# Performance work log

Hardware: AMD Instinct MI355X
Metric: run time of the kernel (lower is better)

Reference implementation:

```python
import jax, jax.numpy as jnp
import numpy as np

B, N, C, K, TOPK = 16, 4096, 256, 8, 2
EPS = 1e-6
RATIO = 0.1      # gate_geno_ratio
TEMP = 1.0       # gate_temperature


def setup_inputs() -> dict:
    key = jax.random.key(0)
    ks = jax.random.split(key, 8)
    s = np.float32(1.0 / np.sqrt(C))  # ~xavier scale for C->C linears
    return {
        "tokens": jax.random.normal(ks[0], (B, N, C), jnp.float32),
        "geno_vec": jax.random.normal(ks[1], (B, C), jnp.float32),
        # gate params (gate_proj init std=0.001; gate_geno given small random instead of exact-zero init so it contributes)
        "Wg": jax.random.normal(ks[2], (K, C), jnp.float32) * 0.001,
        "bg": jnp.zeros((K,), jnp.float32),
        "Wgg": jax.random.normal(ks[3], (K, C), jnp.float32) * 0.001,
        "bgg": jnp.zeros((K,), jnp.float32),
        # per-expert 2-layer MLP params (dropout inactive in eval)
        "W1": jax.random.normal(ks[4], (K, C, C), jnp.float32) * s,
        "b1": jnp.zeros((K, C), jnp.float32),
        "W2": jax.random.normal(ks[5], (K, C, C), jnp.float32) * s,
        "b2": jnp.zeros((K, C), jnp.float32),
    }


def reference(tokens, geno_vec, Wg, bg, Wgg, bgg, W1, b1, W2, b2):
    # gate logits: [B,N,K]
    logits = jnp.einsum("bnc,kc->bnk", tokens, Wg) + bg
    logits = logits + RATIO * (geno_vec @ Wgg.T + bgg)[:, None, :]
    logits = logits / TEMP

    topv, topi = jax.lax.top_k(logits, TOPK)          # [B,N,TOPK]
    topw = jax.nn.softmax(topv, axis=-1)
    topw = jnp.maximum(topw, EPS)
    topw = topw / topw.sum(-1, keepdims=True)

    # dense gate weight matrix W: [B,N,K] (scatter of topw at topi; topk indices are distinct)
    hot = jax.nn.one_hot(topi, K, dtype=tokens.dtype)  # [B,N,TOPK,K]
    Wmat = (hot * topw[..., None]).sum(-2)             # [B,N,K]

    # load-balance loss on hard usage (detached in original)
    usage = jax.lax.stop_gradient(hot.sum(-2).mean((0, 1)))  # [K]
    lb_loss = (jnp.std(usage) / (usage.mean() + EPS)) ** 2

    mass_sum = Wmat.sum(axis=1)                        # [B,K]

    # per-expert MLP computed densely over all tokens; zero gate weight kills
    # non-routed tokens exactly (same math as gather->MLP->scatter-add)
    def expert_center(k):
        h = jax.nn.relu(tokens @ W1[k].T + b1[k])      # [B,N,C]
        out = h @ W2[k].T + b2[k]                      # [B,N,C]
        return jnp.einsum("bn,bnc->bc", Wmat[:, :, k], out)

    centers_sum = jnp.stack([expert_center(k) for k in range(K)], axis=1)  # [B,K,C]
    centers = centers_sum / jnp.maximum(mass_sum, EPS)[..., None]

    routing_confidence = (topv[:, :, 0] - topv[:, :, 1]).mean()
    return centers, lb_loss, routing_confidence
```

## Files before the change

### kernel.cpp

```cpp
#include <hip/hip_runtime.h>

#define B_ 16
#define N_ 4096
#define C_ 256
#define K_ 8
#define EPS 1e-6f
#define RATIO 0.1f

typedef float f32x4 __attribute__((ext_vector_type(4)));
typedef __bf16 bf16x8 __attribute__((ext_vector_type(8)));

__device__ inline unsigned short f2bf(float f){
  unsigned int u = __float_as_uint(f);
  u += 0x7FFFu + ((u >> 16) & 1u);
  return (unsigned short)(u >> 16);
}
__device__ inline float bf2f(unsigned short h){
  return __uint_as_float(((unsigned int)h) << 16);
}

union BFu { ushort4 u4[2]; bf16x8 v; };

__global__ __launch_bounds__(256) void k0_prep(
    const float* __restrict__ W1, const float* __restrict__ Wg,
    const float* __restrict__ geno, const float* __restrict__ Wgg,
    const float* __restrict__ bgg,
    unsigned short* __restrict__ W1swz,
    unsigned short* __restrict__ Wgp_hi, unsigned short* __restrict__ Wgp_lo,
    int* __restrict__ cnt,
    float* __restrict__ mass, float* __restrict__ conf,
    float* __restrict__ glog)
{
  int gid = blockIdx.x * 256 + threadIdx.x;
  if (gid < B_*K_) { cnt[gid] = 0; mass[gid] = 0.f; }
  if (gid == 0) conf[0] = 0.f;
  {
    int o = gid << 3;
    int lane6 = (o >> 3) & 63;
    int s  = (o >> 9) & 7;
    int nt = (o >> 12) & 15;
    int k  = o >> 16;
    int quad = lane6 >> 4, l16 = lane6 & 15;
    int j  = nt*16 + l16;
    int c0 = s*32 + quad*8;
    const float* src = W1 + (k << 16) + (j << 8) + c0;
    unsigned short* dst = W1swz + o;
    #pragma unroll
    for (int e = 0; e < 8; ++e) dst[e] = f2bf(src[e]);
  }
  if (gid < 16*C_){
    int r = gid >> 8, c = gid & 255;
    float v = (r < K_) ? Wg[(r << 8) + c] : 0.f;
    unsigned short h = f2bf(v);
    Wgp_hi[gid] = h;
    Wgp_lo[gid] = f2bf(v - bf2f(h));
  }
  int wv = gid >> 6;
  if (wv < B_*K_){
    int lane = threadIdx.x & 63;
    int b = wv >> 3, k = wv & 7;
    float4 a = *(const float4*)(geno + b*C_ + lane*4);
    float4 w = *(const float4*)(Wgg  + k*C_ + lane*4);
    float p = a.x*w.x + a.y*w.y + a.z*w.z + a.w*w.w;
    #pragma unroll
    for (int off = 32; off; off >>= 1) p += __shfl_xor(p, off);
    if (lane == 0) glog[wv] = RATIO * (p + bgg[k]);
  }
}

__global__ __launch_bounds__(256) void k1_gate(
    const float* __restrict__ tokens,
    const unsigned short* __restrict__ Wgp_hi, const unsigned short* __restrict__ Wgp_lo,
    const float* __restrict__ bg, const float* __restrict__ glog,
    int* __restrict__ cnt, int* __restrict__ bidx, float* __restrict__ bw,
    float* __restrict__ mass, float* __restrict__ conf,
    unsigned short* __restrict__ tok_bf)
{
  __shared__ float ls[64][9];
  __shared__ float bg_s[K_], gl_s[K_], mass_s[K_];
  __shared__ int lcnt[K_], gbase[K_];
  __shared__ int e0s[64], e1s[64], s0s[64], s1s[64];
  __shared__ float w0s[64], w1s[64];
  __shared__ float cred[4];
  int tid = threadIdx.x, lane = tid & 63, wave = tid >> 6;
  int quad = lane >> 4, l16 = lane & 15;
  int b = blockIdx.x >> 6;
  int tok0 = (blockIdx.x & 63) * 64;
  if (tid < K_){ bg_s[tid] = bg[tid]; gl_s[tid] = glog[b*K_ + tid];
                 mass_s[tid] = 0.f; lcnt[tid] = 0; }
  __syncthreads();

  {
    int trow = tok0 + wave*16 + l16;
    const float* xsrc = tokens + ((size_t)b*N_ + trow)*C_ + quad*8;
    unsigned short* bdst = tok_bf + (((size_t)(b*N_ + trow)) << 8) + quad*8;
    float4 xa[8], xb[8];
    #pragma unroll
    for (int s = 0; s < 8; ++s){
      xa[s] = *(const float4*)(xsrc + s*32);
      xb[s] = *(const float4*)(xsrc + s*32 + 4);
    }
    f32x4 acc; acc.x = 0.f; acc.y = 0.f; acc.z = 0.f; acc.w = 0.f;
    #pragma unroll
    for (int s = 0; s < 8; ++s){
      BFu hi, lo;
      hi.u4[0].x = f2bf(xa[s].x); hi.u4[0].y = f2bf(xa[s].y);
      hi.u4[0].z = f2bf(xa[s].z); hi.u4[0].w = f2bf(xa[s].w);
      hi.u4[1].x = f2bf(xb[s].x); hi.u4[1].y = f2bf(xb[s].y);
      hi.u4[1].z = f2bf(xb[s].z); hi.u4[1].w = f2bf(xb[s].w);
      lo.u4[0].x = f2bf(xa[s].x - bf2f(hi.u4[0].x));
      lo.u4[0].y = f2bf(xa[s].y - bf2f(hi.u4[0].y));
      lo.u4[0].z = f2bf(xa[s].z - bf2f(hi.u4[0].z));
      lo.u4[0].w = f2bf(xa[s].w - bf2f(hi.u4[0].w));
      lo.u4[1].x = f2bf(xb[s].x - bf2f(hi.u4[1].x));
      lo.u4[1].y = f2bf(xb[s].y - bf2f(hi.u4[1].y));
      lo.u4[1].z = f2bf(xb[s].z - bf2f(hi.u4[1].z));
      lo.u4[1].w = f2bf(xb[s].w - bf2f(hi.u4[1].w));
      *(ushort4*)(bdst + s*32)     = hi.u4[0];
      *(ushort4*)(bdst + s*32 + 4) = hi.u4[1];
      bf16x8 bhi = *(const bf16x8*)(Wgp_hi + l16*C_ + s*32 + quad*8);
      bf16x8 blo = *(const bf16x8*)(Wgp_lo + l16*C_ + s*32 + quad*8);
      acc = __builtin_amdgcn_mfma_f32_16x16x32_bf16(hi.v, bhi, acc, 0, 0, 0);
      acc = __builtin_amdgcn_mfma_f32_16x16x32_bf16(lo.v, bhi, acc, 0, 0, 0);
      acc = __builtin_amdgcn_mfma_f32_16x16x32_bf16(hi.v, blo, acc, 0, 0, 0);
    }
    if (l16 < K_){
      #pragma unroll
      for (int rr = 0; rr < 4; ++rr){
        int tl = wave*16 + quad*4 + rr;
        ls[tl][l16] = acc[rr] + bg_s[l16] + gl_s[l16];
      }
    }
  }
  __syncthreads();

  if (quad == 0){
    int t = (wave << 4) | l16;
    float v0 = -1e30f, v1 = -1e30f; int i0 = 0, i1 = 0;
    #pragma unroll
    for (int kk = 0; kk < K_; ++kk){
      float l = ls[t][kk];
      if (l > v0){ v1 = v0; i1 = i0; v0 = l; i0 = kk; }
      else if (l > v1){ v1 = l; i1 = kk; }
    }
    float e  = expf(v1 - v0);
    float w0 = 1.f / (1.f + e), w1 = e / (1.f + e);
    w0 = fmaxf(w0, EPS); w1 = fmaxf(w1, EPS);
    float inv = 1.f / (w0 + w1);
    w0 *= inv; w1 *= inv;
    int p0 = atomicAdd(&lcnt[i0], 1);
    int p1 = atomicAdd(&lcnt[i1], 1);
    e0s[t] = i0; e1s[t] = i1; s0s[t] = p0; s1s[t] = p1;
    w0s[t] = w0; w1s[t] = w1;
    atomicAdd(&mass_s[i0], w0);
    atomicAdd(&mass_s[i1], w1);
    float ca = v0 - v1;
    #pragma unroll
    for (int off = 8; off; off >>= 1) ca += __shfl_down(ca, off);
    if (l16 == 0) cred[wave] = ca;
  }
  __syncthreads();
  if (tid < K_){
    gbase[tid] = atomicAdd(&cnt[b*K_ + tid], lcnt[tid]);
    atomicAdd(&mass[b*K_ + tid], mass_s[tid]);
  }
  if (tid == 0) atomicAdd(conf, cred[0] + cred[1] + cred[2] + cred[3]);
  __syncthreads();
  if (quad == 0){
    int t = (wave << 4) | l16;
    int n = tok0 + t;
    int ke0 = e0s[t], ke1 = e1s[t];
    size_t o0 = (size_t)(b*K_ + ke0)*N_ + gbase[ke0] + s0s[t];
    size_t o1 = (size_t)(b*K_ + ke1)*N_ + gbase[ke1] + s1s[t];
    bidx[o0] = n;  bw[o0] = w0s[t];
    bidx[o1] = n;  bw[o1] = w1s[t];
  }
}

#define K4_STAGE(T, REG) do {                                                  \
    _Pragma("unroll")                                                          \
    for (int i = 0; i < 2; ++i){                                               \
      int c16 = (T)*512 + i*256 + tid;                                         \
      __builtin_amdgcn_global_load_lds(                                        \
        (const __attribute__((address_space(1))) unsigned int*)(wsrc + c16*8), \
        (__attribute__((address_space(3))) unsigned int*)(&Bs[REG][0] + (i*256 + tid)*8), \
        16, 0, 0);                                                             \
    }                                                                          \
  } while(0)

__global__ __launch_bounds__(256, 3) void k4_expert(
    const unsigned short* __restrict__ tok_bf, const unsigned short* __restrict__ W1swz,
    const float* __restrict__ b1, const int* __restrict__ cnt,
    const int* __restrict__ bidx, const float* __restrict__ bw,
    float* __restrict__ gpart)
{
  int lin = blockIdx.x;
  int halfg = lin >> 11;
  int l2i = lin & 2047;
  int w = (halfg << 11) | ((l2i & 7) << 8) | (l2i >> 3);
  int bat = w >> 8;
  int k = (w >> 5) & 7;
  int chunk = w & 31;
  int bucket = (bat << 3) | k;
  int M = cnt[bucket];
  if (chunk * 128 >= M) return;
  int Mm1 = M - 1;

  __shared__ unsigned short Bs[6][4096];
  __shared__ float wtok[128];
  __shared__ float red[2][4][16];

  int tid = threadIdx.x, lane = tid & 63, wave = tid >> 6;
  int quad = lane >> 4, l16 = lane & 15;
  int bwbase = bucket << 12;

  const unsigned short* wsrc = W1swz + ((size_t)k << 16);

  K4_STAGE(0, 0);
  K4_STAGE(1, 1);
  K4_STAGE(2, 2);

  if (tid < 128){
    int tn = chunk*128 + tid;
    wtok[tid] = (tn < M) ? bw[bwbase + tn] : 0.f;
  }

  int r0 = chunk*128 + (wave << 4) + l16;
  int nn0 = bidx[bwbase + min(r0, Mm1)];
  int nn1 = bidx[bwbase + min(r0 + 64, Mm1)];
  const unsigned short* p0 = tok_bf + (((size_t)((bat << 12) + nn0)) << 8) + (quad << 3);
  const unsigned short* p1 = tok_bf + (((size_t)((bat << 12) + nn1)) << 8) + (quad << 3);
  bf16x8 a0[8], a1[8];
  #pragma unroll
  for (int s = 0; s < 8; ++s){
    a0[s] = *(const bf16x8*)(p0 + s*32);
    a1[s] = *(const bf16x8*)(p1 + s*32);
  }

  float bias[16];
  #pragma unroll
  for (int p = 0; p < 16; ++p) bias[p] = b1[(k << 8) + (p << 4) + l16];

  float* gdst = gpart + (size_t)(((bucket << 5) + chunk) << 8);
  int wq = (wave << 4) + (quad << 2);

  #pragma unroll
  for (int p = 0; p < 16; ++p){
    if (p <= 12) K4_STAGE(p + 3, (p + 3) % 6);
    if (p <= 12){
      asm volatile("s_waitcnt vmcnt(6) lgkmcnt(0)" ::: "memory");
    } else if (p == 13){
      asm volatile("s_waitcnt vmcnt(4) lgkmcnt(0)" ::: "memory");
    } else if (p == 14){
      asm volatile("s_waitcnt vmcnt(2) lgkmcnt(0)" ::: "memory");
    } else {
      asm volatile("s_waitcnt vmcnt(0) lgkmcnt(0)" ::: "memory");
    }
    __builtin_amdgcn_s_barrier();

    if (p > 0 && tid < 16){
      int pb = (p - 1) & 1;
      float sv = red[pb][0][tid] + red[pb][1][tid]
               + red[pb][2][tid] + red[pb][3][tid];
      gdst[((p - 1) << 4) + tid] = sv;
    }

    f32x4 acc0, acc1;
    acc0.x=0.f; acc0.y=0.f; acc0.z=0.f; acc0.w=0.f;
    acc1.x=0.f; acc1.y=0.f; acc1.z=0.f; acc1.w=0.f;
    #pragma unroll
    for (int s = 0; s < 8; ++s){
      bf16x8 bb = *(const bf16x8*)(&Bs[p % 6][0] + ((s*64 + lane) << 3));
      acc0 = __builtin_amdgcn_mfma_f32_16x16x32_bf16(a0[s], bb, acc0, 0, 0, 0);
      acc1 = __builtin_amdgcn_mfma_f32_16x16x32_bf16(a1[s], bb, acc1, 0, 0, 0);
    }
    float pt = 0.f;
    #pragma unroll
    for (int rr = 0; rr < 4; ++rr){
      float h0 = fmaxf(acc0[rr] + bias[p], 0.f);
      float h1 = fmaxf(acc1[rr] + bias[p], 0.f);
      pt += wtok[wq + rr] * h0 + wtok[64 + wq + rr] * h1;
    }
    pt += __shfl_down(pt, 32);
    pt += __shfl_down(pt, 16);
    if (lane < 16) red[p & 1][wave][lane] = pt;
  }
  asm volatile("s_waitcnt lgkmcnt(0)" ::: "memory");
  __builtin_amdgcn_s_barrier();
  if (tid < 16){
    float sv = red[1][0][tid] + red[1][1][tid] + red[1][2][tid] + red[1][3][tid];
    gdst[(15 << 4) + tid] = sv;
  }
}

__global__ __launch_bounds__(256) void k5_centers(
    const float* __restrict__ gpart, const int* __restrict__ cnt,
    const float* __restrict__ W2, const float* __restrict__ b2,
    const float* __restrict__ mass, const float* __restrict__ conf,
    float* __restrict__ out)
{
  __shared__ float gv[C_];
  int z = blockIdx.x, tid = threadIdx.x;
  int k = z & 7;
  int nch = (cnt[z] + 127) >> 7;
  float sv = 0.f;
  for (int c = 0; c < nch; ++c)
    sv += gpart[(size_t)((((z << 5) + c) << 8) + tid)];
  gv[tid] = sv;
  __syncthreads();
  float m = mass[z];
  float inv = 1.f / fmaxf(m, EPS);
  int tq = tid & 3, cb = tid >> 2;
  #pragma unroll 1
  for (int h = 0; h < 2; ++h){
    int c = (blockIdx.y*2 + h)*64 + cb;
    const float4* wrow = (const float4*)(W2 + ((((k << 8) + c)) << 8));
    float dot = 0.f;
    #pragma unroll
    for (int jj = 0; jj < 16; ++jj){
      float4 w4 = wrow[jj*4 + tq];
      float4 g4 = *(const float4*)&gv[(jj*4 + tq) * 4];
      dot += w4.x*g4.x + w4.y*g4.y + w4.z*g4.z + w4.w*g4.w;
    }
    dot += __shfl_xor(dot, 1);
    dot += __shfl_xor(dot, 2);
    if (tq == 0) out[z*C_ + c] = (dot + m * b2[k*C_ + c]) * inv;
  }
  if (z == 0 && blockIdx.y == 0 && tid == 0){
    float u[K_];
    #pragma unroll
    for (int kk = 0; kk < K_; ++kk) u[kk] = 0.f;
    for (int i = 0; i < B_*K_; ++i) u[i & 7] += (float)cnt[i];
    float mean = 0.f;
    #pragma unroll
    for (int kk = 0; kk < K_; ++kk){ u[kk] *= (1.f / (float)(B_*N_)); mean += u[kk]; }
    mean *= (1.f / K_);
    float var = 0.f;
    #pragma unroll
    for (int kk = 0; kk < K_; ++kk){ float d = u[kk] - mean; var += d*d; }
    var *= (1.f / K_);
    float denom = mean + EPS;
    out[B_*K_*C_]     = var / (denom * denom);
    out[B_*K_*C_ + 1] = conf[0] / (float)(B_*N_);
  }
}

extern "C" void kernel_launch(void* const* d_in, const int* in_sizes, int n_in,
                              void* d_out, int out_size, void* d_ws, size_t ws_size,
                              hipStream_t stream)
{
  const float* tokens = (const float*)d_in[0];
  const float* geno   = (const float*)d_in[1];
  const float* Wg     = (const float*)d_in[2];
  const float* bg     = (const float*)d_in[3];
  const float* Wgg    = (const float*)d_in[4];
  const float* bgg    = (const float*)d_in[5];
  const float* W1     = (const float*)d_in[6];
  const float* b1     = (const float*)d_in[7];
  const float* W2     = (const float*)d_in[8];
  const float* b2     = (const float*)d_in[9];
  float* out = (float*)d_out;
  char* ws = (char*)d_ws;
  unsigned short* W1swz  = (unsigned short*)(ws);
  unsigned short* Wgp_hi = (unsigned short*)(ws + 1048576);
  unsigned short* Wgp_lo = (unsigned short*)(ws + 1056768);
  float* glog = (float*)(ws + 1196032);
  int*   cnt  = (int*)  (ws + 1196544);
  float* mass = (float*)(ws + 1197056);
  float* conf = (float*)(ws + 1197568);
  int*   bidx = (int*)  (ws + 1198080);
  float* bw   = (float*)(ws + 3295232);
  unsigned short* tok_bf = (unsigned short*)(ws + 5392384);
  float* gpart = (float*)(ws + 38946816);

  k0_prep<<<256, 256, 0, stream>>>(W1, Wg, geno, Wgg, bgg, W1swz, Wgp_hi, Wgp_lo,
                                   cnt, mass, conf, glog);
  k1_gate<<<1024, 256, 0, stream>>>(tokens, Wgp_hi, Wgp_lo, bg, glog,
                                    cnt, bidx, bw, mass, conf, tok_bf);
  k4_expert<<<4096, 256, 0, stream>>>(tok_bf, W1swz, b1, cnt, bidx, bw, gpart);
  k5_centers<<<dim3(128, 2), 256, 0, stream>>>(gpart, cnt, W2, b2, mass, conf, out);
}
```

Baseline: 181.4 us.

## Compact expert grid via prefix-sum chunk mapping and shallower LDS pipeline

The expert kernel now computes a prefix sum over per-bucket chunk counts in each block and maps blocks to only the live (bucket, chunk) pairs with a binary search. This replaces the fixed 4096-block grid, most of whose blocks exited early, with 1152 blocks. The weight staging ring shrinks from 6 to 4 LDS buffers so that 4 blocks per CU can fit. The gate kernel also adds asm register barriers that force all token loads to be issued before conversion. The risks are a shallower prefetch depth, extra scan work per block, and failure if the chunk total ever exceeds 1152 (top-2 of 8 experts bounds it at about 1152).

```diff
diff --git a/kernel.cpp b/kernel.cpp
--- a/kernel.cpp
+++ b/kernel.cpp
@@ -94,28 +94,32 @@
     int trow = tok0 + wave*16 + l16;
     const float* xsrc = tokens + ((size_t)b*N_ + trow)*C_ + quad*8;
     unsigned short* bdst = tok_bf + (((size_t)(b*N_ + trow)) << 8) + quad*8;
-    float4 xa[8], xb[8];
+    f32x4 xa[8], xb[8];
     #pragma unroll
     for (int s = 0; s < 8; ++s){
-      xa[s] = *(const float4*)(xsrc + s*32);
-      xb[s] = *(const float4*)(xsrc + s*32 + 4);
-    }
+      xa[s] = *(const f32x4*)(xsrc + s*32);
+      xb[s] = *(const f32x4*)(xsrc + s*32 + 4);
+    }
+    asm volatile("" : "+v"(xa[0]), "+v"(xa[1]), "+v"(xa[2]), "+v"(xa[3]),
+                      "+v"(xa[4]), "+v"(xa[5]), "+v"(xa[6]), "+v"(xa[7]));
+    asm volatile("" : "+v"(xb[0]), "+v"(xb[1]), "+v"(xb[2]), "+v"(xb[3]),
+                      "+v"(xb[4]), "+v"(xb[5]), "+v"(xb[6]), "+v"(xb[7]));
     f32x4 acc; acc.x = 0.f; acc.y = 0.f; acc.z = 0.f; acc.w = 0.f;
     #pragma unroll
     for (int s = 0; s < 8; ++s){
       BFu hi, lo;
-      hi.u4[0].x = f2bf(xa[s].x); hi.u4[0].y = f2bf(xa[s].y);
-      hi.u4[0].z = f2bf(xa[s].z); hi.u4[0].w = f2bf(xa[s].w);
-      hi.u4[1].x = f2bf(xb[s].x); hi.u4[1].y = f2bf(xb[s].y);
-      hi.u4[1].z = f2bf(xb[s].z); hi.u4[1].w = f2bf(xb[s].w);
-      lo.u4[0].x = f2bf(xa[s].x - bf2f(hi.u4[0].x));
-      lo.u4[0].y = f2bf(xa[s].y - bf2f(hi.u4[0].y));
-      lo.u4[0].z = f2bf(xa[s].z - bf2f(hi.u4[0].z));
-      lo.u4[0].w = f2bf(xa[s].w - bf2f(hi.u4[0].w));
-      lo.u4[1].x = f2bf(xb[s].x - bf2f(hi.u4[1].x));
-      lo.u4[1].y = f2bf(xb[s].y - bf2f(hi.u4[1].y));
-      lo.u4[1].z = f2bf(xb[s].z - bf2f(hi.u4[1].z));
-      lo.u4[1].w = f2bf(xb[s].w - bf2f(hi.u4[1].w));
+      hi.u4[0].x = f2bf(xa[s][0]); hi.u4[0].y = f2bf(xa[s][1]);
+      hi.u4[0].z = f2bf(xa[s][2]); hi.u4[0].w = f2bf(xa[s][3]);
+      hi.u4[1].x = f2bf(xb[s][0]); hi.u4[1].y = f2bf(xb[s][1]);
+      hi.u4[1].z = f2bf(xb[s][2]); hi.u4[1].w = f2bf(xb[s][3]);
+      lo.u4[0].x = f2bf(xa[s][0] - bf2f(hi.u4[0].x));
+      lo.u4[0].y = f2bf(xa[s][1] - bf2f(hi.u4[0].y));
+      lo.u4[0].z = f2bf(xa[s][2] - bf2f(hi.u4[0].z));
+      lo.u4[0].w = f2bf(xa[s][3] - bf2f(hi.u4[0].w));
+      lo.u4[1].x = f2bf(xb[s][0] - bf2f(hi.u4[1].x));
+      lo.u4[1].y = f2bf(xb[s][1] - bf2f(hi.u4[1].y));
+      lo.u4[1].z = f2bf(xb[s][2] - bf2f(hi.u4[1].z));
+      lo.u4[1].w = f2bf(xb[s][3] - bf2f(hi.u4[1].w));
       *(ushort4*)(bdst + s*32)     = hi.u4[0];
       *(ushort4*)(bdst + s*32 + 4) = hi.u4[1];
       bf16x8 bhi = *(const bf16x8*)(Wgp_hi + l16*C_ + s*32 + quad*8);
@@ -188,37 +192,58 @@
     }                                                                          \
   } while(0)
 
-__global__ __launch_bounds__(256, 3) void k4_expert(
+__global__ __launch_bounds__(256, 4) void k4_expert(
     const unsigned short* __restrict__ tok_bf, const unsigned short* __restrict__ W1swz,
     const float* __restrict__ b1, const int* __restrict__ cnt,
     const int* __restrict__ bidx, const float* __restrict__ bw,
     float* __restrict__ gpart)
 {
-  int lin = blockIdx.x;
-  int halfg = lin >> 11;
-  int l2i = lin & 2047;
-  int w = (halfg << 11) | ((l2i & 7) << 8) | (l2i >> 3);
-  int bat = w >> 8;
-  int k = (w >> 5) & 7;
-  int chunk = w & 31;
-  int bucket = (bat << 3) | k;
-  int M = cnt[bucket];
-  if (chunk * 128 >= M) return;
-  int Mm1 = M - 1;
-
-  __shared__ unsigned short Bs[6][4096];
+  __shared__ unsigned short Bs[4][4096];
   __shared__ float wtok[128];
   __shared__ float red[2][4][16];
+  __shared__ int Pb[129];
 
   int tid = threadIdx.x, lane = tid & 63, wave = tid >> 6;
   int quad = lane >> 4, l16 = lane & 15;
+
+  if (wave == 0){
+    int b2i = lane << 1;
+    int cA = (cnt[b2i] + 127) >> 7;
+    int cB = (cnt[b2i + 1] + 127) >> 7;
+    int s = cA + cB;
+    int ps = s;
+    #pragma unroll
+    for (int off = 1; off < 64; off <<= 1){
+      int t = __shfl_up(ps, off);
+      if (lane >= off) ps += t;
+    }
+    Pb[b2i]     = ps - s;
+    Pb[b2i + 1] = ps - cB;
+    if (lane == 63) Pb[128] = ps;
+  }
+  __syncthreads();
+
+  int T = Pb[128];
+  int lin = blockIdx.x;
+  int wq = (lin & 7) * 144 + (lin >> 3);
+  if (wq >= T) return;
+  int lo = 0, hi = 128;
+  #pragma unroll
+  for (int it = 0; it < 7; ++it){
+    int mid = (lo + hi) >> 1;
+    if (Pb[mid] <= wq) lo = mid; else hi = mid;
+  }
+  int bucket = lo;
+  int chunk = wq - Pb[lo];
+  int bat = bucket >> 3, k = bucket & 7;
+  int M = cnt[bucket];
+  int Mm1 = M - 1;
   int bwbase = bucket << 12;
 
   const unsigned short* wsrc = W1swz + ((size_t)k << 16);
 
   K4_STAGE(0, 0);
   K4_STAGE(1, 1);
-  K4_STAGE(2, 2);
 
   if (tid < 128){
     int tn = chunk*128 + tid;
@@ -242,14 +267,12 @@
   for (int p = 0; p < 16; ++p) bias[p] = b1[(k << 8) + (p << 4) + l16];
 
   float* gdst = gpart + (size_t)(((bucket << 5) + chunk) << 8);
-  int wq = (wave << 4) + (quad << 2);
+  int wq4 = (wave << 4) + (quad << 2);
 
   #pragma unroll
   for (int p = 0; p < 16; ++p){
-    if (p <= 12) K4_STAGE(p + 3, (p + 3) % 6);
-    if (p <= 12){
-      asm volatile("s_waitcnt vmcnt(6) lgkmcnt(0)" ::: "memory");
-    } else if (p == 13){
+    if (p < 14){
+      K4_STAGE(p + 2, (p + 2) & 3);
       asm volatile("s_waitcnt vmcnt(4) lgkmcnt(0)" ::: "memory");
     } else if (p == 14){
       asm volatile("s_waitcnt vmcnt(2) lgkmcnt(0)" ::: "memory");
@@ -270,7 +293,7 @@
     acc1.x=0.f; acc1.y=0.f; acc1.z=0.f; acc1.w=0.f;
     #pragma unroll
     for (int s = 0; s < 8; ++s){
-      bf16x8 bb = *(const bf16x8*)(&Bs[p % 6][0] + ((s*64 + lane) << 3));
+      bf16x8 bb = *(const bf16x8*)(&Bs[p & 3][0] + ((s*64 + lane) << 3));
       acc0 = __builtin_amdgcn_mfma_f32_16x16x32_bf16(a0[s], bb, acc0, 0, 0, 0);
       acc1 = __builtin_amdgcn_mfma_f32_16x16x32_bf16(a1[s], bb, acc1, 0, 0, 0);
     }
@@ -279,7 +302,7 @@
     for (int rr = 0; rr < 4; ++rr){
       float h0 = fmaxf(acc0[rr] + bias[p], 0.f);
       float h1 = fmaxf(acc1[rr] + bias[p], 0.f);
-      pt += wtok[wq + rr] * h0 + wtok[64 + wq + rr] * h1;
+      pt += wtok[wq4 + rr] * h0 + wtok[64 + wq4 + rr] * h1;
     }
     pt += __shfl_down(pt, 32);
     pt += __shfl_down(pt, 16);
@@ -377,6 +400,6 @@
                                    cnt, mass, conf, glog);
   k1_gate<<<1024, 256, 0, stream>>>(tokens, Wgp_hi, Wgp_lo, bg, glog,
                                     cnt, bidx, bw, mass, conf, tok_bf);
-  k4_expert<<<4096, 256, 0, stream>>>(tok_bf, W1swz, b1, cnt, bidx, bw, gpart);
+  k4_expert<<<1152, 256, 0, stream>>>(tok_bf, W1swz, b1, cnt, bidx, bw, gpart);
   k5_centers<<<dim3(128, 2), 256, 0, stream>>>(gpart, cnt, W2, b2, mass, conf, out);
 }
```

Result: no change. 178.7 us (-1.5%).
